# Performance work log

Hardware: AMD Instinct MI355X
Metric: run time of the kernel (lower is better)

## Reference

```python
import jax, jax.numpy as jnp
import numpy as np

B, N, DIM, H, D = 4, 2048, 1024, 16, 64  # inner_dim = dim // n_heads
NEG_INF = float('-inf')


def setup_inputs() -> dict:
    key = jax.random.key(0)
    k1, k2, k3, k4 = jax.random.split(key, 4)
    x = jax.random.normal(k1, (B, N, DIM), dtype=jnp.float32)
    Wqkv = jax.random.normal(k2, (3 * H * D, DIM), dtype=jnp.float32) * (DIM ** -0.5)
    key_mask = jax.random.randint(k3, (B, N), 0, 2).astype(jnp.bool_)
    query_mask = jax.random.randint(k4, (B, N), 0, 2).astype(jnp.bool_)
    return {"x": x, "Wqkv": Wqkv, "key_mask": key_mask, "query_mask": query_mask, "causal": 1}


def reference(x, Wqkv, key_mask, query_mask, causal):
    # fused qkv projection (self-attention fast path)
    qkv = jnp.einsum('bnc,fc->bnf', x, Wqkv)  # [B, N, 3*H*D]
    q, k, v = jnp.split(qkv, 3, axis=-1)
    def to_heads(t):
        return t.reshape(B, N, H, D).transpose(0, 2, 1, 3)  # b h n d
    q, k, v = to_heads(q), to_heads(k), to_heads(v)

    attn = jnp.einsum('bhnd,bhmd->bhnm', q, k) / np.sqrt(D).astype(np.float32)

    # pairwise key/query mask: [B, 1, Nq, Nk]
    pair = key_mask[:, None, None, :] & query_mask[:, None, :, None]
    attn = attn + jnp.where(pair, 0.0, NEG_INF)

    if causal:
        causal_mask = jnp.triu(jnp.full((N, N), NEG_INF, dtype=attn.dtype), k=1)
        attn = attn + causal_mask

    attn = jax.nn.softmax(attn, axis=-1)
    attn = jnp.nan_to_num(attn, nan=0.0)  # fully-masked rows -> 0

    out = jnp.einsum('bhnm,bhmd->bhnd', attn, v)
    out = out.transpose(0, 2, 1, 3).reshape(B, N, H * D)  # b n (h d)
    # inner_dim * n_heads == dim, so out_proj is skipped (matches torch code)
    return out
```

## Files before the change

### kernel.cpp

```cpp
#include <hip/hip_runtime.h>
#include <hip/hip_bf16.h>

typedef unsigned short u16;
typedef __attribute__((ext_vector_type(8))) short bf16x8;
typedef __attribute__((ext_vector_type(4))) float f32x4;

#define Bdim 4
#define Nseq 2048
#define DIMc 1024
#define NH   16
#define HD   64
#define F3   3072
#define Mrows 8192

static __device__ __forceinline__ u16 f2b(float f) {
    union { float f; unsigned u; } v; v.f = f;
    unsigned r = v.u + 0x7fffu + ((v.u >> 16) & 1u);
    return (u16)(r >> 16);
}

__global__ __launch_bounds__(256) void cast_f32_bf16_kernel(const float* __restrict__ in,
                                                            u16* __restrict__ out, int n4) {
    int i = blockIdx.x * 256 + threadIdx.x;
    if (i >= n4) return;
    float4 v = reinterpret_cast<const float4*>(in)[i];
    ushort4 o;
    o.x = f2b(v.x); o.y = f2b(v.y); o.z = f2b(v.z); o.w = f2b(v.w);
    reinterpret_cast<ushort4*>(out)[i] = o;
}

__global__ __launch_bounds__(256) void norm_mask_kernel(const void* __restrict__ raw, int n,
                                                        int* __restrict__ outm) {
    const unsigned* as_u = (const unsigned*)raw;
    const float* as_f = (const float*)raw;
    const unsigned char* as_b = (const unsigned char*)raw;
    int ns = n < 512 ? n : 512;
    bool ok_i = true, ok_f = true;
    for (int i = 0; i < ns; ++i) {
        unsigned v = as_u[i];
        ok_i &= (v <= 1u);
        ok_f &= (v == 0u) || (v == 0x3f800000u);
    }
    const int mode = ok_i ? 0 : (ok_f ? 1 : 2);
    int i = blockIdx.x * 256 + threadIdx.x;
    if (i < n) {
        int v;
        if (mode == 0) v = (int)as_u[i];
        else if (mode == 1) v = (as_f[i] != 0.f) ? 1 : 0;
        else v = (int)as_b[i];
        outm[i] = (v != 0) ? 1 : 0;
    }
}

__global__ __launch_bounds__(256, 2) void qkv_gemm_kernel(const u16* __restrict__ A,
                                                          const u16* __restrict__ Bw,
                                                          u16* __restrict__ C) {
    __shared__ u16 As[128][72];
    __shared__ u16 Bs[128][72];
    const int t = threadIdx.x;
    const int lane = t & 63;
    const int wave = t >> 6;
    const int wr = (wave >> 1) * 64;
    const int wc = (wave & 1) * 64;
    const int row0 = blockIdx.x * 128;
    const int col0 = blockIdx.y * 128;

    const int lr = lane & 15;
    const int lk = (lane >> 4) * 8;
    const int cr = (lane >> 4) * 4;
    const int cc = lane & 15;

    const f32x4 fzero = {0.f, 0.f, 0.f, 0.f};
    f32x4 acc[4][4];
#pragma unroll
    for (int i = 0; i < 4; ++i)
#pragma unroll
        for (int j = 0; j < 4; ++j) acc[i][j] = fzero;

    const int strow = t >> 3;
    const int stcol = (t & 7) * 8;

    for (int k0 = 0; k0 < DIMc; k0 += 64) {
        __syncthreads();
#pragma unroll
        for (int it = 0; it < 4; ++it) {
            const int r = it * 32 + strow;
            *reinterpret_cast<bf16x8*>(&As[r][stcol]) =
                *reinterpret_cast<const bf16x8*>(A + (size_t)(row0 + r) * DIMc + k0 + stcol);
            *reinterpret_cast<bf16x8*>(&Bs[r][stcol]) =
                *reinterpret_cast<const bf16x8*>(Bw + (size_t)(col0 + r) * DIMc + k0 + stcol);
        }
        __syncthreads();

        bf16x8 af[4][2], bfr[4][2];
#pragma unroll
        for (int i = 0; i < 4; ++i)
#pragma unroll
            for (int ks = 0; ks < 2; ++ks) {
                af[i][ks]  = *reinterpret_cast<const bf16x8*>(&As[wr + i * 16 + lr][ks * 32 + lk]);
                bfr[i][ks] = *reinterpret_cast<const bf16x8*>(&Bs[wc + i * 16 + lr][ks * 32 + lk]);
            }
#pragma unroll
        for (int ks = 0; ks < 2; ++ks)
#pragma unroll
            for (int mi = 0; mi < 4; ++mi)
#pragma unroll
                for (int ni = 0; ni < 4; ++ni)
                    acc[mi][ni] = __builtin_amdgcn_mfma_f32_16x16x32_bf16(af[mi][ks], bfr[ni][ks], acc[mi][ni], 0, 0, 0);
    }

#pragma unroll
    for (int mi = 0; mi < 4; ++mi)
#pragma unroll
        for (int ni = 0; ni < 4; ++ni)
#pragma unroll
            for (int j = 0; j < 4; ++j) {
                int r = row0 + wr + mi * 16 + cr + j;
                int c = col0 + wc + ni * 16 + cc;
                C[(size_t)r * F3 + c] = f2b(acc[mi][ni][j]);
            }
}

__global__ __launch_bounds__(256, 2) void attn_kernel(const u16* __restrict__ qkv,
                                                      const int* __restrict__ key_mask,
                                                      const int* __restrict__ query_mask,
                                                      const int* __restrict__ causal_p,
                                                      float* __restrict__ out) {
    const int bh = blockIdx.x;
    const int qt = blockIdx.y;
    const int b = bh >> 4;
    const int h = bh & 15;
    const int t = threadIdx.x;
    const int lane = t & 63;
    const int wave = t >> 6;
    const int g = lane >> 4;
    const int lq = lane & 15;
    const int causal = causal_p[0];

    __shared__ u16 Ks[64][72];
    __shared__ u16 Vt[64][72];
    __shared__ u16 Ps[4][32][72];

    const int q0 = qt * 128;
    const int wq0 = q0 + wave * 32;

    const f32x4 fzero = {0.f, 0.f, 0.f, 0.f};

    bf16x8 qfr[2][2];
#pragma unroll
    for (int qf = 0; qf < 2; ++qf)
#pragma unroll
        for (int ks = 0; ks < 2; ++ks)
            qfr[qf][ks] = *reinterpret_cast<const bf16x8*>(
                qkv + (size_t)(b * Nseq + wq0 + qf * 16 + lq) * F3 + h * HD + ks * 32 + g * 8);

    int qmv[2];
    float mrow[2], lsum[2];
    f32x4 oacc[4][2];
#pragma unroll
    for (int qf = 0; qf < 2; ++qf) {
        qmv[qf] = query_mask[b * Nseq + wq0 + qf * 16 + lq];
        mrow[qf] = -1e30f;
        lsum[qf] = 0.f;
    }
#pragma unroll
    for (int df = 0; df < 4; ++df)
#pragma unroll
        for (int qf = 0; qf < 2; ++qf) oacc[df][qf] = fzero;

    const int kvend = causal ? (q0 + 128) : Nseq;
    const int sr = t >> 2;
    const int sc = (t & 3) * 8;

    for (int m0 = 0; m0 < kvend; m0 += 64) {
        const u16* krow = qkv + (size_t)(b * Nseq + m0 + sr) * F3 + DIMc + h * HD;
        *reinterpret_cast<bf16x8*>(&Ks[sr][sc])      = *reinterpret_cast<const bf16x8*>(krow + sc);
        *reinterpret_cast<bf16x8*>(&Ks[sr][sc + 32]) = *reinterpret_cast<const bf16x8*>(krow + sc + 32);
        {
            const u16* vrow = qkv + (size_t)(b * Nseq + m0 + lane) * F3 + 2 * DIMc + h * HD + wave * 16;
            bf16x8 v0 = *reinterpret_cast<const bf16x8*>(vrow);
            bf16x8 v1 = *reinterpret_cast<const bf16x8*>(vrow + 8);
#pragma unroll
            for (int e = 0; e < 8; ++e) {
                Vt[wave * 16 + e][lane]     = (u16)v0[e];
                Vt[wave * 16 + 8 + e][lane] = (u16)v1[e];
            }
        }
        __syncthreads();

        f32x4 sacc[4][2];
#pragma unroll
        for (int kf = 0; kf < 4; ++kf)
#pragma unroll
            for (int qf = 0; qf < 2; ++qf) sacc[kf][qf] = fzero;
        bf16x8 ka[4][2];
#pragma unroll
        for (int kf = 0; kf < 4; ++kf)
#pragma unroll
            for (int ks = 0; ks < 2; ++ks)
                ka[kf][ks] = *reinterpret_cast<const bf16x8*>(&Ks[kf * 16 + lq][ks * 32 + g * 8]);
#pragma unroll
        for (int kf = 0; kf < 4; ++kf)
#pragma unroll
            for (int qf = 0; qf < 2; ++qf) {
                sacc[kf][qf] = __builtin_amdgcn_mfma_f32_16x16x32_bf16(ka[kf][0], qfr[qf][0], sacc[kf][qf], 0, 0, 0);
                sacc[kf][qf] = __builtin_amdgcn_mfma_f32_16x16x32_bf16(ka[kf][1], qfr[qf][1], sacc[kf][qf], 0, 0, 0);
            }

        int4 km4[4];
#pragma unroll
        for (int kf = 0; kf < 4; ++kf)
            km4[kf] = *reinterpret_cast<const int4*>(key_mask + b * Nseq + m0 + kf * 16 + g * 4);

#pragma unroll
        for (int qf = 0; qf < 2; ++qf) {
            const int qg = wq0 + qf * 16 + lq;
            const bool qok = (qmv[qf] != 0);
            float s[4][4];
            float mx = -1e30f;
#pragma unroll
            for (int kf = 0; kf < 4; ++kf) {
                const int* kmr = reinterpret_cast<const int*>(&km4[kf]);
#pragma unroll
                for (int r = 0; r < 4; ++r) {
                    const int kg = m0 + kf * 16 + g * 4 + r;
                    float sv = sacc[kf][qf][r] * 0.125f;
                    const bool ok = qok && (kmr[r] != 0) && (!causal || kg <= qg);
                    sv = ok ? sv : -1e30f;
                    s[kf][r] = sv;
                    mx = fmaxf(mx, sv);
                }
            }
            mx = fmaxf(mx, __shfl_xor(mx, 16));
            mx = fmaxf(mx, __shfl_xor(mx, 32));
            const float mnew = fmaxf(mrow[qf], mx);
            const float scale = __expf(mrow[qf] - mnew);
            float rs = 0.f;
#pragma unroll
            for (int kf = 0; kf < 4; ++kf)
#pragma unroll
                for (int r = 0; r < 4; ++r) {
                    const float pv = (s[kf][r] > -1e29f) ? __expf(s[kf][r] - mnew) : 0.f;
                    s[kf][r] = pv;
                    rs += pv;
                }
            rs += __shfl_xor(rs, 16);
            rs += __shfl_xor(rs, 32);
            lsum[qf] = lsum[qf] * scale + rs;
            mrow[qf] = mnew;
#pragma unroll
            for (int df = 0; df < 4; ++df) oacc[df][qf] *= scale;
#pragma unroll
            for (int kf = 0; kf < 4; ++kf)
#pragma unroll
                for (int r = 0; r < 4; ++r)
                    Ps[wave][qf * 16 + lq][kf * 16 + g * 4 + r] = f2b(s[kf][r]);
        }

        bf16x8 va[4][2], pb[2][2];
#pragma unroll
        for (int df = 0; df < 4; ++df)
#pragma unroll
            for (int kc = 0; kc < 2; ++kc)
                va[df][kc] = *reinterpret_cast<const bf16x8*>(&Vt[df * 16 + lq][kc * 32 + g * 8]);
#pragma unroll
        for (int qf = 0; qf < 2; ++qf)
#pragma unroll
            for (int kc = 0; kc < 2; ++kc)
                pb[qf][kc] = *reinterpret_cast<const bf16x8*>(&Ps[wave][qf * 16 + lq][kc * 32 + g * 8]);
#pragma unroll
        for (int df = 0; df < 4; ++df)
#pragma unroll
            for (int qf = 0; qf < 2; ++qf) {
                oacc[df][qf] = __builtin_amdgcn_mfma_f32_16x16x32_bf16(va[df][0], pb[qf][0], oacc[df][qf], 0, 0, 0);
                oacc[df][qf] = __builtin_amdgcn_mfma_f32_16x16x32_bf16(va[df][1], pb[qf][1], oacc[df][qf], 0, 0, 0);
            }
        __syncthreads();
    }

#pragma unroll
    for (int qf = 0; qf < 2; ++qf) {
        const float inv = (mrow[qf] > -1e29f && lsum[qf] > 0.f) ? 1.f / lsum[qf] : 0.f;
        const size_t rowoff = (size_t)(b * Nseq + wq0 + qf * 16 + lq) * DIMc + h * HD;
#pragma unroll
        for (int df = 0; df < 4; ++df)
#pragma unroll
            for (int r = 0; r < 4; ++r)
                out[rowoff + df * 16 + g * 4 + r] = oacc[df][qf][r] * inv;
    }
}

extern "C" void kernel_launch(void* const* d_in, const int* in_sizes, int n_in,
                              void* d_out, int out_size, void* d_ws, size_t ws_size,
                              hipStream_t stream) {
    const float* x = (const float*)d_in[0];
    const float* W = (const float*)d_in[1];

    char* ws = (char*)d_ws;
    int* km_n = (int*)(ws);
    int* qm_n = (int*)(ws + 32 * 1024);
    int* ca_n = (int*)(ws + 64 * 1024);
    u16* qkv  = (u16*)(ws + (size_t)1024 * 1024);
    u16* xb   = (u16*)(ws + (size_t)49 * 1024 * 1024);
    u16* wb   = (u16*)(ws + (size_t)65 * 1024 * 1024);

    const int nm = Bdim * Nseq;
    norm_mask_kernel<<<(nm + 255) / 256, 256, 0, stream>>>(d_in[2], nm, km_n);
    norm_mask_kernel<<<(nm + 255) / 256, 256, 0, stream>>>(d_in[3], nm, qm_n);
    norm_mask_kernel<<<1, 256, 0, stream>>>(d_in[4], 1, ca_n);

    const int nx4 = (Mrows * DIMc) / 4;
    const int nw4 = (F3 * DIMc) / 4;
    cast_f32_bf16_kernel<<<(nx4 + 255) / 256, 256, 0, stream>>>(x, xb, nx4);
    cast_f32_bf16_kernel<<<(nw4 + 255) / 256, 256, 0, stream>>>(W, wb, nw4);

    qkv_gemm_kernel<<<dim3(Mrows / 128, F3 / 128), 256, 0, stream>>>(xb, wb, qkv);

    attn_kernel<<<dim3(Bdim * NH, Nseq / 128), 256, 0, stream>>>(qkv, km_n, qm_n, ca_n,
                                                                 (float*)d_out);
}
```

Before: 268.9 us.

## Pair causal query tiles per block, prefetch K/V, use direct-to-LDS loads in GEMM

The attention kernel now gives each block two query tiles (p and 15-p) so every block does the same amount of causal work, and the two tiles share each loaded K/V tile. The next K/V tile is prefetched into registers while the current one is computed. The QKV GEMM switches to global_load_lds direct-to-LDS loads with a K-step of 32 and an unpadded LDS layout. In exchange, register pressure rises in attention and the unpadded GEMM LDS layout may cause bank conflicts. The p/15-p pairing also assumes causal mode: when causal is off, both tiles are still processed correctly, but the work-balancing benefit is lost.

```diff
diff --git a/kernel.cpp b/kernel.cpp
--- a/kernel.cpp
+++ b/kernel.cpp
@@ -12,6 +12,9 @@
 #define HD   64
 #define F3   3072
 #define Mrows 8192
+
+typedef const __attribute__((address_space(1))) unsigned int gl_u32;
+typedef __attribute__((address_space(3))) unsigned int lds_u32;
 
 static __device__ __forceinline__ u16 f2b(float f) {
     union { float f; unsigned u; } v; v.f = f;
@@ -55,8 +58,8 @@
 __global__ __launch_bounds__(256, 2) void qkv_gemm_kernel(const u16* __restrict__ A,
                                                           const u16* __restrict__ Bw,
                                                           u16* __restrict__ C) {
-    __shared__ u16 As[128][72];
-    __shared__ u16 Bs[128][72];
+    __shared__ u16 As[128 * 32];
+    __shared__ u16 Bs[128 * 32];
     const int t = threadIdx.x;
     const int lane = t & 63;
     const int wave = t >> 6;
@@ -77,36 +80,34 @@
 #pragma unroll
         for (int j = 0; j < 4; ++j) acc[i][j] = fzero;
 
-    const int strow = t >> 3;
-    const int stcol = (t & 7) * 8;
-
-    for (int k0 = 0; k0 < DIMc; k0 += 64) {
+    const int strow = wave * 16 + (lane >> 2);
+    const int stcol = (lane & 3) * 8;
+
+    for (int k0 = 0; k0 < DIMc; k0 += 32) {
         __syncthreads();
 #pragma unroll
-        for (int it = 0; it < 4; ++it) {
-            const int r = it * 32 + strow;
-            *reinterpret_cast<bf16x8*>(&As[r][stcol]) =
-                *reinterpret_cast<const bf16x8*>(A + (size_t)(row0 + r) * DIMc + k0 + stcol);
-            *reinterpret_cast<bf16x8*>(&Bs[r][stcol]) =
-                *reinterpret_cast<const bf16x8*>(Bw + (size_t)(col0 + r) * DIMc + k0 + stcol);
+        for (int issue = 0; issue < 2; ++issue) {
+            const int r = issue * 64 + strow;
+            __builtin_amdgcn_global_load_lds(
+                (gl_u32*)(A + (size_t)(row0 + r) * DIMc + k0 + stcol),
+                (lds_u32*)(As + (size_t)(issue * 64 + wave * 16) * 32), 16, 0, 0);
+            __builtin_amdgcn_global_load_lds(
+                (gl_u32*)(Bw + (size_t)(col0 + r) * DIMc + k0 + stcol),
+                (lds_u32*)(Bs + (size_t)(issue * 64 + wave * 16) * 32), 16, 0, 0);
         }
         __syncthreads();
 
-        bf16x8 af[4][2], bfr[4][2];
-#pragma unroll
-        for (int i = 0; i < 4; ++i)
-#pragma unroll
-            for (int ks = 0; ks < 2; ++ks) {
-                af[i][ks]  = *reinterpret_cast<const bf16x8*>(&As[wr + i * 16 + lr][ks * 32 + lk]);
-                bfr[i][ks] = *reinterpret_cast<const bf16x8*>(&Bs[wc + i * 16 + lr][ks * 32 + lk]);
-            }
-#pragma unroll
-        for (int ks = 0; ks < 2; ++ks)
-#pragma unroll
-            for (int mi = 0; mi < 4; ++mi)
-#pragma unroll
-                for (int ni = 0; ni < 4; ++ni)
-                    acc[mi][ni] = __builtin_amdgcn_mfma_f32_16x16x32_bf16(af[mi][ks], bfr[ni][ks], acc[mi][ni], 0, 0, 0);
+        bf16x8 af[4], bfr[4];
+#pragma unroll
+        for (int i = 0; i < 4; ++i) {
+            af[i]  = *reinterpret_cast<const bf16x8*>(&As[(wr + i * 16 + lr) * 32 + lk]);
+            bfr[i] = *reinterpret_cast<const bf16x8*>(&Bs[(wc + i * 16 + lr) * 32 + lk]);
+        }
+#pragma unroll
+        for (int mi = 0; mi < 4; ++mi)
+#pragma unroll
+            for (int ni = 0; ni < 4; ++ni)
+                acc[mi][ni] = __builtin_amdgcn_mfma_f32_16x16x32_bf16(af[mi], bfr[ni], acc[mi][ni], 0, 0, 0);
     }
 
 #pragma unroll
@@ -119,6 +120,86 @@
                 int c = col0 + wc + ni * 16 + cc;
                 C[(size_t)r * F3 + c] = f2b(acc[mi][ni][j]);
             }
+}
+
+static __device__ __forceinline__ void attn_tile_compute(
+    const bf16x8 (&qfr)[2][2], const int (&qmv)[2],
+    float (&mrow)[2], float (&lsum)[2], f32x4 (&oacc)[4][2],
+    const bf16x8 (&ka)[4][2], const bf16x8 (&va)[4][2],
+    const int (&km)[4][4],
+    int wq0, int m0, int causal,
+    u16 (*Psw)[72], int g, int lq)
+{
+    const f32x4 fzero = {0.f, 0.f, 0.f, 0.f};
+    f32x4 sacc[4][2];
+#pragma unroll
+    for (int kf = 0; kf < 4; ++kf)
+#pragma unroll
+        for (int qf = 0; qf < 2; ++qf) sacc[kf][qf] = fzero;
+#pragma unroll
+    for (int kf = 0; kf < 4; ++kf)
+#pragma unroll
+        for (int qf = 0; qf < 2; ++qf) {
+            sacc[kf][qf] = __builtin_amdgcn_mfma_f32_16x16x32_bf16(ka[kf][0], qfr[qf][0], sacc[kf][qf], 0, 0, 0);
+            sacc[kf][qf] = __builtin_amdgcn_mfma_f32_16x16x32_bf16(ka[kf][1], qfr[qf][1], sacc[kf][qf], 0, 0, 0);
+        }
+
+#pragma unroll
+    for (int qf = 0; qf < 2; ++qf) {
+        const int qg = wq0 + qf * 16 + lq;
+        const bool qok = (qmv[qf] != 0);
+        float s[4][4];
+        float mx = -1e30f;
+#pragma unroll
+        for (int kf = 0; kf < 4; ++kf)
+#pragma unroll
+            for (int r = 0; r < 4; ++r) {
+                const int kg = m0 + kf * 16 + g * 4 + r;
+                float sv = sacc[kf][qf][r] * 0.125f;
+                const bool ok = qok && (km[kf][r] != 0) && (!causal || kg <= qg);
+                sv = ok ? sv : -1e30f;
+                s[kf][r] = sv;
+                mx = fmaxf(mx, sv);
+            }
+        mx = fmaxf(mx, __shfl_xor(mx, 16));
+        mx = fmaxf(mx, __shfl_xor(mx, 32));
+        const float mnew = fmaxf(mrow[qf], mx);
+        const float scale = __expf(mrow[qf] - mnew);
+        float rs = 0.f;
+#pragma unroll
+        for (int kf = 0; kf < 4; ++kf)
+#pragma unroll
+            for (int r = 0; r < 4; ++r) {
+                const float pv = (s[kf][r] > -1e29f) ? __expf(s[kf][r] - mnew) : 0.f;
+                s[kf][r] = pv;
+                rs += pv;
+            }
+        rs += __shfl_xor(rs, 16);
+        rs += __shfl_xor(rs, 32);
+        lsum[qf] = lsum[qf] * scale + rs;
+        mrow[qf] = mnew;
+#pragma unroll
+        for (int df = 0; df < 4; ++df) oacc[df][qf] *= scale;
+#pragma unroll
+        for (int kf = 0; kf < 4; ++kf)
+#pragma unroll
+            for (int r = 0; r < 4; ++r)
+                Psw[qf * 16 + lq][kf * 16 + g * 4 + r] = f2b(s[kf][r]);
+    }
+
+    bf16x8 pb[2][2];
+#pragma unroll
+    for (int qf = 0; qf < 2; ++qf)
+#pragma unroll
+        for (int kc = 0; kc < 2; ++kc)
+            pb[qf][kc] = *reinterpret_cast<const bf16x8*>(&Psw[qf * 16 + lq][kc * 32 + g * 8]);
+#pragma unroll
+    for (int df = 0; df < 4; ++df)
+#pragma unroll
+        for (int qf = 0; qf < 2; ++qf) {
+            oacc[df][qf] = __builtin_amdgcn_mfma_f32_16x16x32_bf16(va[df][0], pb[qf][0], oacc[df][qf], 0, 0, 0);
+            oacc[df][qf] = __builtin_amdgcn_mfma_f32_16x16x32_bf16(va[df][1], pb[qf][1], oacc[df][qf], 0, 0, 0);
+        }
 }
 
 __global__ __launch_bounds__(256, 2) void attn_kernel(const u16* __restrict__ qkv,
@@ -127,7 +208,7 @@
                                                       const int* __restrict__ causal_p,
                                                       float* __restrict__ out) {
     const int bh = blockIdx.x;
-    const int qt = blockIdx.y;
+    const int p = blockIdx.y;
     const int b = bh >> 4;
     const int h = bh & 15;
     const int t = threadIdx.x;
@@ -141,152 +222,113 @@
     __shared__ u16 Vt[64][72];
     __shared__ u16 Ps[4][32][72];
 
-    const int q0 = qt * 128;
-    const int wq0 = q0 + wave * 32;
+    const int q0A = p * 128;
+    const int q0B = (15 - p) * 128;
+    const int wq0A = q0A + wave * 32;
+    const int wq0B = q0B + wave * 32;
 
     const f32x4 fzero = {0.f, 0.f, 0.f, 0.f};
 
-    bf16x8 qfr[2][2];
+    bf16x8 qfrA[2][2], qfrB[2][2];
 #pragma unroll
     for (int qf = 0; qf < 2; ++qf)
 #pragma unroll
-        for (int ks = 0; ks < 2; ++ks)
-            qfr[qf][ks] = *reinterpret_cast<const bf16x8*>(
-                qkv + (size_t)(b * Nseq + wq0 + qf * 16 + lq) * F3 + h * HD + ks * 32 + g * 8);
-
-    int qmv[2];
-    float mrow[2], lsum[2];
-    f32x4 oacc[4][2];
+        for (int ks = 0; ks < 2; ++ks) {
+            qfrA[qf][ks] = *reinterpret_cast<const bf16x8*>(
+                qkv + (size_t)(b * Nseq + wq0A + qf * 16 + lq) * F3 + h * HD + ks * 32 + g * 8);
+            qfrB[qf][ks] = *reinterpret_cast<const bf16x8*>(
+                qkv + (size_t)(b * Nseq + wq0B + qf * 16 + lq) * F3 + h * HD + ks * 32 + g * 8);
+        }
+
+    int qmA[2], qmB[2];
+    float mrowA[2], lsumA[2], mrowB[2], lsumB[2];
+    f32x4 oaccA[4][2], oaccB[4][2];
 #pragma unroll
     for (int qf = 0; qf < 2; ++qf) {
-        qmv[qf] = query_mask[b * Nseq + wq0 + qf * 16 + lq];
-        mrow[qf] = -1e30f;
-        lsum[qf] = 0.f;
+        qmA[qf] = query_mask[b * Nseq + wq0A + qf * 16 + lq];
+        qmB[qf] = query_mask[b * Nseq + wq0B + qf * 16 + lq];
+        mrowA[qf] = -1e30f; lsumA[qf] = 0.f;
+        mrowB[qf] = -1e30f; lsumB[qf] = 0.f;
     }
 #pragma unroll
     for (int df = 0; df < 4; ++df)
 #pragma unroll
-        for (int qf = 0; qf < 2; ++qf) oacc[df][qf] = fzero;
-
-    const int kvend = causal ? (q0 + 128) : Nseq;
+        for (int qf = 0; qf < 2; ++qf) { oaccA[df][qf] = fzero; oaccB[df][qf] = fzero; }
+
+    const int kvendA = causal ? (q0A + 128) : Nseq;
+    const int kvendB = causal ? (q0B + 128) : Nseq;
+
     const int sr = t >> 2;
     const int sc = (t & 3) * 8;
 
-    for (int m0 = 0; m0 < kvend; m0 += 64) {
-        const u16* krow = qkv + (size_t)(b * Nseq + m0 + sr) * F3 + DIMc + h * HD;
-        *reinterpret_cast<bf16x8*>(&Ks[sr][sc])      = *reinterpret_cast<const bf16x8*>(krow + sc);
-        *reinterpret_cast<bf16x8*>(&Ks[sr][sc + 32]) = *reinterpret_cast<const bf16x8*>(krow + sc + 32);
-        {
-            const u16* vrow = qkv + (size_t)(b * Nseq + m0 + lane) * F3 + 2 * DIMc + h * HD + wave * 16;
-            bf16x8 v0 = *reinterpret_cast<const bf16x8*>(vrow);
-            bf16x8 v1 = *reinterpret_cast<const bf16x8*>(vrow + 8);
-#pragma unroll
-            for (int e = 0; e < 8; ++e) {
-                Vt[wave * 16 + e][lane]     = (u16)v0[e];
-                Vt[wave * 16 + 8 + e][lane] = (u16)v1[e];
-            }
+    bf16x8 kr0, kr1, vr0, vr1;
+    {
+        const u16* krow = qkv + (size_t)(b * Nseq + 0 + sr) * F3 + DIMc + h * HD;
+        kr0 = *reinterpret_cast<const bf16x8*>(krow + sc);
+        kr1 = *reinterpret_cast<const bf16x8*>(krow + sc + 32);
+        const u16* vrow = qkv + (size_t)(b * Nseq + 0 + lane) * F3 + 2 * DIMc + h * HD + wave * 16;
+        vr0 = *reinterpret_cast<const bf16x8*>(vrow);
+        vr1 = *reinterpret_cast<const bf16x8*>(vrow + 8);
+    }
+
+    for (int m0 = 0; m0 < kvendB; m0 += 64) {
+        *reinterpret_cast<bf16x8*>(&Ks[sr][sc])      = kr0;
+        *reinterpret_cast<bf16x8*>(&Ks[sr][sc + 32]) = kr1;
+#pragma unroll
+        for (int e = 0; e < 8; ++e) {
+            Vt[wave * 16 + e][lane]     = (u16)vr0[e];
+            Vt[wave * 16 + 8 + e][lane] = (u16)vr1[e];
         }
         __syncthreads();
 
-        f32x4 sacc[4][2];
-#pragma unroll
-        for (int kf = 0; kf < 4; ++kf)
-#pragma unroll
-            for (int qf = 0; qf < 2; ++qf) sacc[kf][qf] = fzero;
-        bf16x8 ka[4][2];
+        if (m0 + 64 < kvendB) {
+            const u16* krow = qkv + (size_t)(b * Nseq + m0 + 64 + sr) * F3 + DIMc + h * HD;
+            kr0 = *reinterpret_cast<const bf16x8*>(krow + sc);
+            kr1 = *reinterpret_cast<const bf16x8*>(krow + sc + 32);
+            const u16* vrow = qkv + (size_t)(b * Nseq + m0 + 64 + lane) * F3 + 2 * DIMc + h * HD + wave * 16;
+            vr0 = *reinterpret_cast<const bf16x8*>(vrow);
+            vr1 = *reinterpret_cast<const bf16x8*>(vrow + 8);
+        }
+
+        int km[4][4];
+#pragma unroll
+        for (int kf = 0; kf < 4; ++kf) {
+            int4 k4 = *reinterpret_cast<const int4*>(key_mask + b * Nseq + m0 + kf * 16 + g * 4);
+            km[kf][0] = k4.x; km[kf][1] = k4.y; km[kf][2] = k4.z; km[kf][3] = k4.w;
+        }
+        bf16x8 ka[4][2], va[4][2];
 #pragma unroll
         for (int kf = 0; kf < 4; ++kf)
 #pragma unroll
             for (int ks = 0; ks < 2; ++ks)
                 ka[kf][ks] = *reinterpret_cast<const bf16x8*>(&Ks[kf * 16 + lq][ks * 32 + g * 8]);
 #pragma unroll
-        for (int kf = 0; kf < 4; ++kf)
-#pragma unroll
-            for (int qf = 0; qf < 2; ++qf) {
-                sacc[kf][qf] = __builtin_amdgcn_mfma_f32_16x16x32_bf16(ka[kf][0], qfr[qf][0], sacc[kf][qf], 0, 0, 0);
-                sacc[kf][qf] = __builtin_amdgcn_mfma_f32_16x16x32_bf16(ka[kf][1], qfr[qf][1], sacc[kf][qf], 0, 0, 0);
-            }
-
-        int4 km4[4];
-#pragma unroll
-        for (int kf = 0; kf < 4; ++kf)
-            km4[kf] = *reinterpret_cast<const int4*>(key_mask + b * Nseq + m0 + kf * 16 + g * 4);
-
-#pragma unroll
-        for (int qf = 0; qf < 2; ++qf) {
-            const int qg = wq0 + qf * 16 + lq;
-            const bool qok = (qmv[qf] != 0);
-            float s[4][4];
-            float mx = -1e30f;
-#pragma unroll
-            for (int kf = 0; kf < 4; ++kf) {
-                const int* kmr = reinterpret_cast<const int*>(&km4[kf]);
-#pragma unroll
-                for (int r = 0; r < 4; ++r) {
-                    const int kg = m0 + kf * 16 + g * 4 + r;
-                    float sv = sacc[kf][qf][r] * 0.125f;
-                    const bool ok = qok && (kmr[r] != 0) && (!causal || kg <= qg);
-                    sv = ok ? sv : -1e30f;
-                    s[kf][r] = sv;
-                    mx = fmaxf(mx, sv);
-                }
-            }
-            mx = fmaxf(mx, __shfl_xor(mx, 16));
-            mx = fmaxf(mx, __shfl_xor(mx, 32));
-            const float mnew = fmaxf(mrow[qf], mx);
-            const float scale = __expf(mrow[qf] - mnew);
-            float rs = 0.f;
-#pragma unroll
-            for (int kf = 0; kf < 4; ++kf)
-#pragma unroll
-                for (int r = 0; r < 4; ++r) {
-                    const float pv = (s[kf][r] > -1e29f) ? __expf(s[kf][r] - mnew) : 0.f;
-                    s[kf][r] = pv;
-                    rs += pv;
-                }
-            rs += __shfl_xor(rs, 16);
-            rs += __shfl_xor(rs, 32);
-            lsum[qf] = lsum[qf] * scale + rs;
-            mrow[qf] = mnew;
-#pragma unroll
-            for (int df = 0; df < 4; ++df) oacc[df][qf] *= scale;
-#pragma unroll
-            for (int kf = 0; kf < 4; ++kf)
-#pragma unroll
-                for (int r = 0; r < 4; ++r)
-                    Ps[wave][qf * 16 + lq][kf * 16 + g * 4 + r] = f2b(s[kf][r]);
-        }
-
-        bf16x8 va[4][2], pb[2][2];
-#pragma unroll
         for (int df = 0; df < 4; ++df)
 #pragma unroll
             for (int kc = 0; kc < 2; ++kc)
                 va[df][kc] = *reinterpret_cast<const bf16x8*>(&Vt[df * 16 + lq][kc * 32 + g * 8]);
-#pragma unroll
-        for (int qf = 0; qf < 2; ++qf)
-#pragma unroll
-            for (int kc = 0; kc < 2; ++kc)
-                pb[qf][kc] = *reinterpret_cast<const bf16x8*>(&Ps[wave][qf * 16 + lq][kc * 32 + g * 8]);
+
+        attn_tile_compute(qfrB, qmB, mrowB, lsumB, oaccB, ka, va, km, wq0B, m0, causal,
+                          Ps[wave], g, lq);
+        if (m0 < kvendA)
+            attn_tile_compute(qfrA, qmA, mrowA, lsumA, oaccA, ka, va, km, wq0A, m0, causal,
+                              Ps[wave], g, lq);
+        __syncthreads();
+    }
+
+#pragma unroll
+    for (int qf = 0; qf < 2; ++qf) {
+        const float invA = (mrowA[qf] > -1e29f && lsumA[qf] > 0.f) ? 1.f / lsumA[qf] : 0.f;
+        const float invB = (mrowB[qf] > -1e29f && lsumB[qf] > 0.f) ? 1.f / lsumB[qf] : 0.f;
+        const size_t rowA = (size_t)(b * Nseq + wq0A + qf * 16 + lq) * DIMc + h * HD;
+        const size_t rowB = (size_t)(b * Nseq + wq0B + qf * 16 + lq) * DIMc + h * HD;
 #pragma unroll
         for (int df = 0; df < 4; ++df)
 #pragma unroll
-            for (int qf = 0; qf < 2; ++qf) {
-                oacc[df][qf] = __builtin_amdgcn_mfma_f32_16x16x32_bf16(va[df][0], pb[qf][0], oacc[df][qf], 0, 0, 0);
-                oacc[df][qf] = __builtin_amdgcn_mfma_f32_16x16x32_bf16(va[df][1], pb[qf][1], oacc[df][qf], 0, 0, 0);
+            for (int r = 0; r < 4; ++r) {
+                out[rowA + df * 16 + g * 4 + r] = oaccA[df][qf][r] * invA;
+                out[rowB + df * 16 + g * 4 + r] = oaccB[df][qf][r] * invB;
             }
-        __syncthreads();
-    }
-
-#pragma unroll
-    for (int qf = 0; qf < 2; ++qf) {
-        const float inv = (mrow[qf] > -1e29f && lsum[qf] > 0.f) ? 1.f / lsum[qf] : 0.f;
-        const size_t rowoff = (size_t)(b * Nseq + wq0 + qf * 16 + lq) * DIMc + h * HD;
-#pragma unroll
-        for (int df = 0; df < 4; ++df)
-#pragma unroll
-            for (int r = 0; r < 4; ++r)
-                out[rowoff + df * 16 + g * 4 + r] = oacc[df][qf][r] * inv;
     }
 }
 
@@ -316,6 +358,6 @@
 
     qkv_gemm_kernel<<<dim3(Mrows / 128, F3 / 128), 256, 0, stream>>>(xb, wb, qkv);
 
-    attn_kernel<<<dim3(Bdim * NH, Nseq / 128), 256, 0, stream>>>(qkv, km_n, qm_n, ca_n,
-                                                                 (float*)d_out);
-}
+    attn_kernel<<<dim3(Bdim * NH, 8), 256, 0, stream>>>(qkv, km_n, qm_n, ca_n,
+                                                        (float*)d_out);
+}
```

Result: faster. 244.0 us (-9.3%).
